# Performance work log

Hardware: AMD Instinct MI355X
Metric: run time of the kernel (lower is better)

The kernel has to match this reference:

```python
import jax, jax.numpy as jnp
import numpy as np

# Module config (matches FootprintExtruder defaults)
L1_HEIGHT = 0
ROOF_HEIGHT = 1
L1_ID_OFFSET = 0
ROOF_ID_OFFSET = 1
FP_ID_MIN = 100
FP_ID_MAX = 5000
MAX_HEIGHT = 384


def setup_inputs() -> dict:
    key = jax.random.key(0)
    k1, k2 = jax.random.split(key)
    B, H, W = 1, 768, 768
    # assert in forward: max(height_field) < max_height
    height_field = jax.random.randint(k1, (B, H, W), 0, MAX_HEIGHT, dtype=jnp.int32)
    seg_map = jax.random.randint(k2, (B, H, W), 0, FP_ID_MAX, dtype=jnp.int32)
    return {"height_field": height_field, "seg_map": seg_map}


def reference(height_field, seg_map):
    """Extrude 2D height/seg maps into a [B, max_height, H, W] voxel id volume.

    For each column (b, h, w) with height hf and id seg:
      z <  hf and seg in footprint_id_range:
          z <  l1_height            -> seg + l1_id_offset
          z >= hf - roof_height     -> seg + roof_id_offset  (roof voxels)
          otherwise                 -> seg
      z <  hf, seg not a footprint  -> seg
      z >= hf                       -> 0 (empty)
    """
    z = jnp.arange(MAX_HEIGHT, dtype=jnp.int32)[None, :, None, None]  # [1, D, 1, 1]
    hf = height_field[:, None, :, :]   # [B, 1, H, W]
    seg = seg_map[:, None, :, :]       # [B, 1, H, W]

    is_fp = (seg >= FP_ID_MIN) & (seg < FP_ID_MAX)
    fp_id = jnp.where(
        z < L1_HEIGHT, seg + L1_ID_OFFSET,
        jnp.where(z >= hf - ROOF_HEIGHT, seg + ROOF_ID_OFFSET, seg),
    )
    volume = jnp.where(z < hf, jnp.where(is_fp, fp_id, seg), 0)
    return volume.astype(jnp.int32)
```

## Files before the change

### kernel.cpp

```cpp
#include <hip/hip_runtime.h>

#define L1_HEIGHT 0
#define ROOF_HEIGHT 1
#define ROOF_ID_OFFSET 1
#define FP_ID_MIN 100
#define FP_ID_MAX 5000
#define MAX_HEIGHT 384
#define HH 768
#define WW 768
#define HW (HH * WW)

typedef int vint4 __attribute__((ext_vector_type(4)));

__device__ __forceinline__ int voxel(int z, int hf, int seg) {
    bool is_fp = (seg >= FP_ID_MIN) & (seg < FP_ID_MAX);
    int fp = (z >= hf - ROOF_HEIGHT) ? seg + ROOF_ID_OFFSET : seg;
    int v  = is_fp ? fp : seg;
    return (z < hf) ? v : 0;
}

__global__ __launch_bounds__(256) void extrude_kernel(
        const int* __restrict__ hf_map, const int* __restrict__ seg_map,
        int* __restrict__ out) {
    const int p = (blockIdx.x * 256 + threadIdx.x) * 4;
    const int z = blockIdx.y;

    const vint4 hf4 = *(const vint4*)(hf_map  + p);
    const vint4 sg4 = *(const vint4*)(seg_map + p);

    vint4 o;
    o.x = voxel(z, hf4.x, sg4.x);
    o.y = voxel(z, hf4.y, sg4.y);
    o.z = voxel(z, hf4.z, sg4.z);
    o.w = voxel(z, hf4.w, sg4.w);

    __builtin_nontemporal_store(o, (vint4*)(out + (size_t)z * HW + p));
}

extern "C" void kernel_launch(void* const* d_in, const int* in_sizes, int n_in,
                              void* d_out, int out_size, void* d_ws, size_t ws_size,
                              hipStream_t stream) {
    const int* hf  = (const int*)d_in[0];
    const int* seg = (const int*)d_in[1];
    int* out = (int*)d_out;

    dim3 grid(HW / 1024, MAX_HEIGHT);
    extrude_kernel<<<grid, 256, 0, stream>>>(hf, seg, out);
}
```

Measured before the change: 841.9 us.

## Process 16 z-slices per thread, precompute roof ids, use regular stores

Result: slower. 862.9 us (+2.5%).

```diff
diff --git a/kernel.cpp b/kernel.cpp
--- a/kernel.cpp
+++ b/kernel.cpp
@@ -1,6 +1,5 @@
 #include <hip/hip_runtime.h>
 
-#define L1_HEIGHT 0
 #define ROOF_HEIGHT 1
 #define ROOF_ID_OFFSET 1
 #define FP_ID_MIN 100
@@ -9,32 +8,37 @@
 #define HH 768
 #define WW 768
 #define HW (HH * WW)
+#define ZPB 16
 
 typedef int vint4 __attribute__((ext_vector_type(4)));
-
-__device__ __forceinline__ int voxel(int z, int hf, int seg) {
-    bool is_fp = (seg >= FP_ID_MIN) & (seg < FP_ID_MAX);
-    int fp = (z >= hf - ROOF_HEIGHT) ? seg + ROOF_ID_OFFSET : seg;
-    int v  = is_fp ? fp : seg;
-    return (z < hf) ? v : 0;
-}
 
 __global__ __launch_bounds__(256) void extrude_kernel(
         const int* __restrict__ hf_map, const int* __restrict__ seg_map,
         int* __restrict__ out) {
-    const int p = (blockIdx.x * 256 + threadIdx.x) * 4;
-    const int z = blockIdx.y;
+    const int p  = (blockIdx.x * 256 + threadIdx.x) * 4;
+    const int z0 = blockIdx.y * ZPB;
 
     const vint4 hf4 = *(const vint4*)(hf_map  + p);
     const vint4 sg4 = *(const vint4*)(seg_map + p);
 
-    vint4 o;
-    o.x = voxel(z, hf4.x, sg4.x);
-    o.y = voxel(z, hf4.y, sg4.y);
-    o.z = voxel(z, hf4.z, sg4.z);
-    o.w = voxel(z, hf4.w, sg4.w);
+    vint4 roof;
+    roof.x = sg4.x + ((sg4.x >= FP_ID_MIN) & (sg4.x < FP_ID_MAX));
+    roof.y = sg4.y + ((sg4.y >= FP_ID_MIN) & (sg4.y < FP_ID_MAX));
+    roof.z = sg4.z + ((sg4.z >= FP_ID_MIN) & (sg4.z < FP_ID_MAX));
+    roof.w = sg4.w + ((sg4.w >= FP_ID_MIN) & (sg4.w < FP_ID_MAX));
 
-    __builtin_nontemporal_store(o, (vint4*)(out + (size_t)z * HW + p));
+    int* outp = out + (size_t)z0 * HW + p;
+    #pragma unroll
+    for (int i = 0; i < ZPB; ++i) {
+        const int z = z0 + i;
+        vint4 o;
+        o.x = (z < hf4.x - 1) ? sg4.x : ((z == hf4.x - 1) ? roof.x : 0);
+        o.y = (z < hf4.y - 1) ? sg4.y : ((z == hf4.y - 1) ? roof.y : 0);
+        o.z = (z < hf4.z - 1) ? sg4.z : ((z == hf4.z - 1) ? roof.z : 0);
+        o.w = (z < hf4.w - 1) ? sg4.w : ((z == hf4.w - 1) ? roof.w : 0);
+        *(vint4*)outp = o;
+        outp += HW;
+    }
 }
 
 extern "C" void kernel_launch(void* const* d_in, const int* in_sizes, int n_in,
@@ -44,6 +48,6 @@
     const int* seg = (const int*)d_in[1];
     int* out = (int*)d_out;
 
-    dim3 grid(HW / 1024, MAX_HEIGHT);
+    dim3 grid(HW / 1024, MAX_HEIGHT / ZPB);
     extrude_kernel<<<grid, 256, 0, stream>>>(hf, seg, out);
 }
```
